# Performance work log

Hardware: AMD Instinct MI355X
Metric: run time of the kernel (lower is better)

Reference implementation:

```python
import jax, jax.numpy as jnp
import numpy as np

N_NODES = 50000
N_EDGES = 800000
NODE_IN = 16
NODE_OUT = 3
H = 128
N_LAYERS = 3


def setup_inputs() -> dict:
    key = jax.random.key(0)
    ks = jax.random.split(key, 16)
    s = 0.05
    inp = {
        "x": jax.random.normal(ks[0], (N_NODES, NODE_IN), dtype=jnp.float32),
        "edge_index": jax.random.randint(ks[1], (2, N_EDGES), 0, N_NODES, dtype=jnp.int64),
        # encoder / decoder
        "enc_w": jax.random.normal(ks[2], (NODE_IN, H), dtype=jnp.float32) * s,
        "enc_b": jnp.zeros((H,), dtype=jnp.float32),
        "dec_w": jax.random.normal(ks[3], (H, NODE_OUT), dtype=jnp.float32) * s,
        "dec_b": jnp.zeros((NODE_OUT,), dtype=jnp.float32),
        # 3 processor layers, edge MLP: Linear(2H,H) -> ReLU -> Linear(H,H)
        "edge_w1": jax.random.normal(ks[4], (N_LAYERS, 2 * H, H), dtype=jnp.float32) * s,
        "edge_b1": jnp.zeros((N_LAYERS, H), dtype=jnp.float32),
        "edge_w2": jax.random.normal(ks[5], (N_LAYERS, H, H), dtype=jnp.float32) * s,
        "edge_b2": jnp.zeros((N_LAYERS, H), dtype=jnp.float32),
        # node MLP: Linear(2H,H) -> ReLU -> Linear(H,H)
        "node_w1": jax.random.normal(ks[6], (N_LAYERS, 2 * H, H), dtype=jnp.float32) * s,
        "node_b1": jnp.zeros((N_LAYERS, H), dtype=jnp.float32),
        "node_w2": jax.random.normal(ks[7], (N_LAYERS, H, H), dtype=jnp.float32) * s,
        "node_b2": jnp.zeros((N_LAYERS, H), dtype=jnp.float32),
    }
    return inp


def reference(x, edge_index, enc_w, enc_b, dec_w, dec_b,
              edge_w1, edge_b1, edge_w2, edge_b2,
              node_w1, node_b1, node_w2, node_b2):
    row = edge_index[0]  # source nodes
    col = edge_index[1]  # destination nodes
    h = x @ enc_w + enc_b  # [N, H]
    for l in range(N_LAYERS):
        # EdgeModel: cat(src, dest) -> MLP
        e_in = jnp.concatenate([h[row], h[col]], axis=1)  # [E, 2H]
        e = jnp.maximum(e_in @ edge_w1[l] + edge_b1[l], 0.0) @ edge_w2[l] + edge_b2[l]  # [E, H]
        # NodeModel: scatter_add messages by col, cat with x -> MLP
        agg = jax.ops.segment_sum(e, col, num_segments=h.shape[0])  # [N, H]
        n_in = jnp.concatenate([h, agg], axis=1)  # [N, 2H]
        h_upd = jnp.maximum(n_in @ node_w1[l] + node_b1[l], 0.0) @ node_w2[l] + node_b2[l]
        h = h + h_upd  # residual
    return h @ dec_w + dec_b  # [N, NODE_OUT]
```

## Files before the change

### kernel.cpp

```cpp
#include <hip/hip_runtime.h>
#include <hip/hip_bf16.h>
#include <stdint.h>

#define N_NODES 50000
#define N_EDGES 800000
#define HID 128
#define NODE_IN 16
#define NODE_OUT 3
#define EDGE_TILES 12500
#define NODE_TILES 782
#define SCAN_BLOCKS 196

typedef __attribute__((ext_vector_type(8))) short short8;
typedef __attribute__((ext_vector_type(4))) float f32x4;

__device__ __forceinline__ unsigned short f2bf(float f) {
    union { float f; unsigned int u; } v; v.f = f;
    unsigned int u = v.u;
    u += 0x7fff + ((u >> 16) & 1);
    return (unsigned short)(u >> 16);
}
__device__ __forceinline__ float bf2f(unsigned short s) {
    union { unsigned int u; float f; } v; v.u = ((unsigned int)s) << 16;
    return v.f;
}
__device__ __forceinline__ float bfu_lo(unsigned int u) {
    union { unsigned int u; float f; } v; v.u = u << 16; return v.f;
}
__device__ __forceinline__ float bfu_hi(unsigned int u) {
    union { unsigned int u; float f; } v; v.u = u & 0xffff0000u; return v.f;
}

__global__ void k1_hist_mfold(const int* __restrict__ colp, int* __restrict__ cnt,
                              int* __restrict__ rank,
                              const float* __restrict__ edge_w2, const float* __restrict__ node_w1,
                              const float* __restrict__ edge_b2,
                              float* __restrict__ Mtmp, float* __restrict__ Vtmp) {
    for (int e = blockIdx.x * 256 + threadIdx.x; e < N_EDGES; e += gridDim.x * 256)
        rank[e] = atomicAdd(&cnt[colp[e]], 1);
    for (int d = blockIdx.x * 256 + threadIdx.x; d < 3 * 16384; d += gridDim.x * 256) {
        int L = d / 16384, rem = d & 16383;
        int k = rem >> 7, n = rem & 127;
        const float* w2  = edge_w2 + (size_t)L * 16384;
        const float* w1b = node_w1 + (size_t)L * 32768 + 16384;
        float acc = 0.f;
        #pragma unroll 4
        for (int j = 0; j < 128; j++) acc += w2[k * 128 + j] * w1b[j * 128 + n];
        Mtmp[d] = acc;
        if (k == 0) {
            const float* b2 = edge_b2 + (size_t)L * 128;
            float vv = 0.f;
            #pragma unroll 4
            for (int j = 0; j < 128; j++) vv += b2[j] * w1b[j * 128 + n];
            Vtmp[L * 128 + n] = vv;
        }
    }
}

__global__ __launch_bounds__(256) void k2a_scan1_swizzle(
    const int* __restrict__ cnt, int* __restrict__ ex, int* __restrict__ bsums,
    const float* __restrict__ edge_w1, const float* __restrict__ node_w1,
    const float* __restrict__ node_w2, const float* __restrict__ Mtmp,
    unsigned short* __restrict__ swz) {
    __shared__ int s[256];
    int b = blockIdx.x, t = threadIdx.x;
    if (b < SCAN_BLOCKS) {
        int i = b * 256 + t;
        int v = (i < N_NODES) ? cnt[i] : 0;
        s[t] = v;
        __syncthreads();
        for (int off = 1; off < 256; off <<= 1) {
            int u = (t >= off) ? s[t - off] : 0;
            __syncthreads();
            s[t] += u;
            __syncthreads();
        }
        if (i < N_NODES) ex[i] = s[t] - v;
        if (t == 255) bsums[b] = s[255];
    } else {
        for (int d = (b - SCAN_BLOCKS) * 256 + t; d < 3 * 98304;
             d += (gridDim.x - SCAN_BLOCKS) * 256) {
            int L = d / 98304;
            int rem = d - L * 98304;
            unsigned short* base = swz + L * 98304;
            if (rem < 32768) {
                const float* w1 = edge_w1 + (size_t)L * 32768;
                int j = rem & 7, ll = (rem >> 3) & 63, tt = rem >> 9;
                int nt = tt & 15, kt = tt >> 4;
                int k = kt * 32 + ((ll >> 4) << 3) + j;
                int cc = nt * 16 + (ll & 15);
                float v = (cc < 128) ? w1[k * 128 + cc] : w1[(128 + k) * 128 + (cc - 128)];
                base[rem] = f2bf(v);
            } else if (rem < 49152) {
            } else if (rem < 81920) {
                int d2 = rem - 49152;
                int j = d2 & 7, ll = (d2 >> 3) & 63, tt = d2 >> 9;
                int nt = tt & 7, kt = tt >> 3;
                int k = kt * 32 + ((ll >> 4) << 3) + j, n = (nt << 4) + (ll & 15);
                float v = (k < 128) ? node_w1[(size_t)L * 32768 + k * 128 + n]
                                    : Mtmp[(size_t)L * 16384 + (k - 128) * 128 + n];
                base[rem] = f2bf(v);
            } else {
                int d2 = rem - 81920;
                const float* src = node_w2 + (size_t)L * 16384;
                int j = d2 & 7, ll = (d2 >> 3) & 63, tt = d2 >> 9;
                int nt = tt & 7, kt = tt >> 3;
                int k = kt * 32 + ((ll >> 4) << 3) + j, n = (nt << 4) + (ll & 15);
                base[rem] = f2bf(src[k * 128 + n]);
            }
        }
    }
}

__global__ void k2b_scan2(int* bsums) {
    __shared__ int s[256];
    int t = threadIdx.x;
    int v = (t < SCAN_BLOCKS) ? bsums[t] : 0;
    s[t] = v;
    __syncthreads();
    for (int off = 1; off < 256; off <<= 1) {
        int u = (t >= off) ? s[t - off] : 0;
        __syncthreads();
        s[t] += u;
        __syncthreads();
    }
    if (t < SCAN_BLOCKS) bsums[t] = s[t] - v;
}

__global__ void k3a_scatter(const int* __restrict__ rowp, const int* __restrict__ colp,
                            const int* __restrict__ ex, const int* __restrict__ bsums,
                            const int* __restrict__ rank, int2* __restrict__ rc_sorted) {
    int e = blockIdx.x * 256 + threadIdx.x;
    if (e >= N_EDGES) return;
    int c = colp[e];
    int pos = ex[c] + bsums[c >> 8] + rank[e];
    rc_sorted[pos] = make_int2(rowp[e], c);
}

__global__ __launch_bounds__(256, 2) void k3b_encoder_sd(
    const float* __restrict__ x, const float* __restrict__ enc_w, const float* __restrict__ enc_b,
    const unsigned short* __restrict__ w1c, unsigned short* __restrict__ h,
    unsigned short* __restrict__ S, unsigned short* __restrict__ D)
{
    __shared__ float wts[NODE_IN * HID];
    __shared__ float bts[HID];
    __shared__ float xs[64][NODE_IN];
    __shared__ unsigned short hs[64][136];
    int t = threadIdx.x, wave = t >> 6, l = t & 63, q = l >> 4, l16 = l & 15;
    int n0 = blockIdx.x * 64;
    int nt0s = wave * 4;

    for (int i = t; i < NODE_IN * HID; i += 256) wts[i] = enc_w[i];
    if (t < HID) bts[t] = enc_b[t];
    for (int i = t; i < 64 * NODE_IN; i += 256) {
        int nl = i >> 4, ii = i & 15;
        int n = n0 + nl;
        xs[nl][ii] = (n < N_NODES) ? x[n * NODE_IN + ii] : 0.f;
    }
    short8 wr[4][4];
    #pragma unroll
    for (int kt = 0; kt < 4; kt++)
        #pragma unroll
        for (int i = 0; i < 4; i++)
            wr[kt][i] = *(const short8*)(w1c + ((kt * 16 + nt0s + i) * 64 + l) * 8);
    __syncthreads();

    for (int o = t; o < 64 * HID; o += 256) {
        int nl = o >> 7, cc = o & 127;
        float acc = bts[cc];
        #pragma unroll
        for (int i = 0; i < NODE_IN; i++) acc += xs[nl][i] * wts[i * HID + cc];
        unsigned short hb = f2bf(acc);
        hs[nl][cc] = hb;
        int n = n0 + nl;
        if (n < N_NODES) h[n * HID + cc] = hb;
    }
    __syncthreads();

    f32x4 acc[4][4];
    #pragma unroll
    for (int g = 0; g < 4; g++)
        #pragma unroll
        for (int i = 0; i < 4; i++) acc[g][i] = (f32x4){0.f, 0.f, 0.f, 0.f};
    #pragma unroll
    for (int kt = 0; kt < 4; kt++) {
        #pragma unroll
        for (int g = 0; g < 4; g++) {
            short8 a = *(const short8*)&hs[g * 16 + l16][kt * 32 + q * 8];
            #pragma unroll
            for (int i = 0; i < 4; i++)
                acc[g][i] = __builtin_amdgcn_mfma_f32_16x16x32_bf16(a, wr[kt][i], acc[g][i], 0, 0, 0);
        }
    }
    #pragma unroll
    for (int i = 0; i < 4; i++) {
        int cc = (nt0s + i) * 16 + l16;
        #pragma unroll
        for (int g = 0; g < 4; g++)
            #pragma unroll
            for (int r = 0; r < 4; r++) {
                int n = n0 + g * 16 + q * 4 + r;
                if (n < N_NODES) {
                    unsigned short v = f2bf(acc[g][i][r]);
                    if (cc < 128) S[n * HID + cc] = v;
                    else          D[n * HID + (cc - 128)] = v;
                }
            }
    }
}

__global__ __launch_bounds__(256, 4) void edge_kernel(
    const unsigned short* __restrict__ S, const unsigned short* __restrict__ D,
    const int2* __restrict__ rc_sorted,
    const float* __restrict__ b1, float* __restrict__ aggH)
{
    __shared__ float hid_s[64][132];
    __shared__ int row_s[64], col_s[64];
    int t = threadIdx.x;
    int ch = t & 15;

    float b1v[8];
    #pragma unroll
    for (int j = 0; j < 8; j++) b1v[j] = b1[ch * 8 + j];

    for (int tile = blockIdx.x; tile < EDGE_TILES; tile += gridDim.x) {
        int e0 = tile * 64;
        if (t < 64) {
            int2 rc = rc_sorted[e0 + t];
            row_s[t] = rc.x;
            col_s[t] = rc.y;
        }
        __syncthreads();

        #pragma unroll
        for (int it = 0; it < 4; it++) {
            int el = it * 16 + (t >> 4);
            int r = row_s[el], c = col_s[el];
            short8 sv = *(const short8*)(S + r * HID + ch * 8);
            short8 dv = *(const short8*)(D + c * HID + ch * 8);
            float o[8];
            #pragma unroll
            for (int p = 0; p < 4; p++) {
                unsigned int us = ((const unsigned int*)&sv)[p];
                unsigned int ud = ((const unsigned int*)&dv)[p];
                float v0 = bfu_lo(us) + bfu_lo(ud) + b1v[p * 2];
                float v1 = bfu_hi(us) + bfu_hi(ud) + b1v[p * 2 + 1];
                o[p * 2]     = v0 > 0.f ? v0 : 0.f;
                o[p * 2 + 1] = v1 > 0.f ? v1 : 0.f;
            }
            *(f32x4*)&hid_s[el][ch * 8]     = *(f32x4*)&o[0];
            *(f32x4*)&hid_s[el][ch * 8 + 4] = *(f32x4*)&o[4];
        }
        __syncthreads();

        {
            int c = t & 127;
            int h2 = t >> 7;
            int r0 = h2 * 32;
            float accv = 0.f;
            int cur = col_s[r0];
            #pragma unroll 4
            for (int r = r0; r < r0 + 32; r++) {
                accv += hid_s[r][c];
                int nxt = (r == r0 + 31) ? -1 : col_s[r + 1];
                if (nxt != cur) {
                    unsafeAtomicAdd(&aggH[cur * HID + c], accv);
                    accv = 0.f;
                    cur = nxt;
                }
            }
        }
        __syncthreads();
    }
}

template<int LAST>
__global__ __launch_bounds__(256, 4) void node_kernel(
    unsigned short* __restrict__ h, float* __restrict__ aggH, const int* __restrict__ cnt,
    const unsigned short* __restrict__ w1m_s, const float* __restrict__ b1,
    const float* __restrict__ vfold,
    const unsigned short* __restrict__ w2s, const float* __restrict__ b2,
    const unsigned short* __restrict__ w1c_next,
    unsigned short* __restrict__ S, unsigned short* __restrict__ D,
    const float* __restrict__ dec_w, const float* __restrict__ dec_b, float* __restrict__ out)
{
    __shared__ unsigned short in_h[64][136];
    __shared__ unsigned short in_a[64][136];
    __shared__ int cnt_s[64];
    __shared__ float dw[HID * NODE_OUT];
    __shared__ float db[NODE_OUT];
    int t = threadIdx.x, wave = t >> 6, l = t & 63, q = l >> 4, l16 = l & 15;
    int nt0 = wave * 2, nt0s = wave * 4;
    int n0 = blockIdx.x * 64;

    if (LAST) {
        for (int i = t; i < HID * NODE_OUT; i += 256) dw[i] = dec_w[i];
        if (t < NODE_OUT) db[t] = dec_b[t];
    }

    #pragma unroll
    for (int it = 0; it < 8; it++) {
        int g = it * 256 + t;
        int nl = g >> 5, sub = g & 31, half = sub >> 4, li = sub & 15;
        int n = n0 + nl;
        short8 v = (short8){0, 0, 0, 0, 0, 0, 0, 0};
        if (n < N_NODES) {
            if (half == 0) {
                v = *(const short8*)(h + n * HID + li * 8);
            } else {
                float* ap = aggH + n * HID + li * 8;
                f32x4 a0 = *(f32x4*)ap, a1 = *(f32x4*)(ap + 4);
                #pragma unroll
                for (int j = 0; j < 4; j++) {
                    ((unsigned short*)&v)[j]     = f2bf(a0[j]);
                    ((unsigned short*)&v)[4 + j] = f2bf(a1[j]);
                }
                if (!LAST) {
                    *(f32x4*)ap       = (f32x4){0.f, 0.f, 0.f, 0.f};
                    *(f32x4*)(ap + 4) = (f32x4){0.f, 0.f, 0.f, 0.f};
                }
            }
        }
        if (half == 0) *(short8*)&in_h[nl][li * 8] = v;
        else           *(short8*)&in_a[nl][li * 8] = v;
    }
    if (t < 64) cnt_s[t] = (n0 + t < N_NODES) ? cnt[n0 + t] : 0;
    __syncthreads();

    float b1r0 = b1[nt0 * 16 + l16], b1r1 = b1[(nt0 + 1) * 16 + l16];
    float vr0 = vfold[nt0 * 16 + l16], vr1 = vfold[(nt0 + 1) * 16 + l16];
    float b2r0 = b2[nt0 * 16 + l16], b2r1 = b2[(nt0 + 1) * 16 + l16];

    f32x4 acc[4][2];
    #pragma unroll
    for (int g = 0; g < 4; g++)
        #pragma unroll
        for (int j = 0; j < 2; j++) acc[g][j] = (f32x4){0.f, 0.f, 0.f, 0.f};
    #pragma unroll
    for (int kt = 0; kt < 8; kt++) {
        short8 b0 = *(const short8*)(w1m_s + ((kt * 8 + nt0)     * 64 + l) * 8);
        short8 b1v = *(const short8*)(w1m_s + ((kt * 8 + nt0 + 1) * 64 + l) * 8);
        #pragma unroll
        for (int g = 0; g < 4; g++) {
            short8 a = (kt < 4) ? *(const short8*)&in_h[g * 16 + l16][kt * 32 + q * 8]
                                : *(const short8*)&in_a[g * 16 + l16][(kt - 4) * 32 + q * 8];
            acc[g][0] = __builtin_amdgcn_mfma_f32_16x16x32_bf16(a, b0, acc[g][0], 0, 0, 0);
            acc[g][1] = __builtin_amdgcn_mfma_f32_16x16x32_bf16(a, b1v, acc[g][1], 0, 0, 0);
        }
    }
    __syncthreads();

    #pragma unroll
    for (int j = 0; j < 2; j++) {
        float bv = j ? b1r1 : b1r0;
        float vv = j ? vr1 : vr0;
        #pragma unroll
        for (int g = 0; g < 4; g++)
            #pragma unroll
            for (int r = 0; r < 4; r++) {
                int m2 = g * 16 + q * 4 + r;
                float v = acc[g][j][r] + bv + (float)cnt_s[m2] * vv;
                v = v > 0.f ? v : 0.f;
                in_a[m2][(nt0 + j) * 16 + l16] = f2bf(v);
            }
    }
    __syncthreads();

    f32x4 acc2[4][2];
    #pragma unroll
    for (int g = 0; g < 4; g++)
        #pragma unroll
        for (int j = 0; j < 2; j++) acc2[g][j] = (f32x4){0.f, 0.f, 0.f, 0.f};
    #pragma unroll
    for (int kt = 0; kt < 4; kt++) {
        short8 b0 = *(const short8*)(w2s + ((kt * 8 + nt0)     * 64 + l) * 8);
        short8 b1v = *(const short8*)(w2s + ((kt * 8 + nt0 + 1) * 64 + l) * 8);
        #pragma unroll
        for (int g = 0; g < 4; g++) {
            short8 a = *(const short8*)&in_a[g * 16 + l16][kt * 32 + q * 8];
            acc2[g][0] = __builtin_amdgcn_mfma_f32_16x16x32_bf16(a, b0, acc2[g][0], 0, 0, 0);
            acc2[g][1] = __builtin_amdgcn_mfma_f32_16x16x32_bf16(a, b1v, acc2[g][1], 0, 0, 0);
        }
    }
    #pragma unroll
    for (int j = 0; j < 2; j++) {
        float bv = j ? b2r1 : b2r0;
        #pragma unroll
        for (int g = 0; g < 4; g++)
            #pragma unroll
            for (int r = 0; r < 4; r++) {
                float v = acc2[g][j][r] + bv;
                int m2 = g * 16 + q * 4 + r;
                int n = n0 + m2;
                if (n < N_NODES) {
                    int c = (nt0 + j) * 16 + l16;
                    unsigned short nh = f2bf(bf2f(in_h[m2][c]) + v);
                    if (!LAST) h[n * HID + c] = nh;
                    in_h[m2][c] = nh;
                }
            }
    }
    __syncthreads();

    if (!LAST) {
        #pragma unroll
        for (int p = 0; p < 2; p++) {
            short8 wr[4][2];
            #pragma unroll
            for (int kt = 0; kt < 4; kt++) {
                wr[kt][0] = *(const short8*)(w1c_next + ((kt * 16 + nt0s + p * 2)     * 64 + l) * 8);
                wr[kt][1] = *(const short8*)(w1c_next + ((kt * 16 + nt0s + p * 2 + 1) * 64 + l) * 8);
            }
            f32x4 accs[4][2];
            #pragma unroll
            for (int g = 0; g < 4; g++)
                #pragma unroll
                for (int i = 0; i < 2; i++) accs[g][i] = (f32x4){0.f, 0.f, 0.f, 0.f};
            #pragma unroll
            for (int kt = 0; kt < 4; kt++) {
                #pragma unroll
                for (int g = 0; g < 4; g++) {
                    short8 a = *(const short8*)&in_h[g * 16 + l16][kt * 32 + q * 8];
                    accs[g][0] = __builtin_amdgcn_mfma_f32_16x16x32_bf16(a, wr[kt][0], accs[g][0], 0, 0, 0);
                    accs[g][1] = __builtin_amdgcn_mfma_f32_16x16x32_bf16(a, wr[kt][1], accs[g][1], 0, 0, 0);
                }
            }
            #pragma unroll
            for (int i = 0; i < 2; i++) {
                int c = (nt0s + p * 2 + i) * 16 + l16;
                #pragma unroll
                for (int g = 0; g < 4; g++)
                    #pragma unroll
                    for (int r = 0; r < 4; r++) {
                        int n = n0 + g * 16 + q * 4 + r;
                        if (n < N_NODES) {
                            unsigned short v = f2bf(accs[g][i][r]);
                            if (c < 128) S[n * HID + c] = v;
                            else         D[n * HID + (c - 128)] = v;
                        }
                    }
            }
        }
    } else {
        if (t < 64 * NODE_OUT) {
            int nl = t / 3, o = t - 3 * nl;
            int n = n0 + nl;
            if (n < N_NODES) {
                float a = db[o];
                #pragma unroll 4
                for (int k = 0; k < HID; k++) a += bf2f(in_h[nl][k]) * dw[k * 3 + o];
                out[n * 3 + o] = a;
            }
        }
    }
}

extern "C" void kernel_launch(void* const* d_in, const int* in_sizes, int n_in,
                              void* d_out, int out_size, void* d_ws, size_t ws_size,
                              hipStream_t stream) {
    const float* x       = (const float*)d_in[0];
    const int*   ei      = (const int*)d_in[1];
    const float* enc_w   = (const float*)d_in[2];
    const float* enc_b   = (const float*)d_in[3];
    const float* dec_w   = (const float*)d_in[4];
    const float* dec_b   = (const float*)d_in[5];
    const float* edge_w1 = (const float*)d_in[6];
    const float* edge_b1 = (const float*)d_in[7];
    const float* edge_w2 = (const float*)d_in[8];
    const float* edge_b2 = (const float*)d_in[9];
    const float* node_w1 = (const float*)d_in[10];
    const float* node_b1 = (const float*)d_in[11];
    const float* node_w2 = (const float*)d_in[12];
    const float* node_b2 = (const float*)d_in[13];

    char* ws = (char*)d_ws;
    unsigned short* h    = (unsigned short*)ws;
    float*          aggH = (float*)(ws + 12800000);
    unsigned short* swz  = (unsigned short*)(ws + 38400000);
    int* cnt             = (int*)(ws + 38989824);
    int* ex              = (int*)(ws + 39189824);
    int* bsums           = (int*)(ws + 39389824);
    int2* rc_sorted      = (int2*)(ws + 39390848);
    unsigned short* Sbuf = (unsigned short*)(ws + 45790848);
    unsigned short* Dbuf = (unsigned short*)(ws + 58590848);
    float* Mtmp          = (float*)(ws + 71390848);
    float* Vtmp          = (float*)(ws + 71587456);
    int* rank            = (int*)(ws + 58590848);

    const int* rowp = ei;
    const int* colp = ei + N_EDGES;

    hipMemsetAsync(cnt, 0, (size_t)N_NODES * 4, stream);
    hipMemsetAsync(aggH, 0, (size_t)N_NODES * HID * 4, stream);

    k1_hist_mfold<<<1024, 256, 0, stream>>>(colp, cnt, rank, edge_w2, node_w1, edge_b2,
                                            Mtmp, Vtmp);
    k2a_scan1_swizzle<<<SCAN_BLOCKS + 288, 256, 0, stream>>>(cnt, ex, bsums, edge_w1,
                                                             node_w1, node_w2, Mtmp, swz);
    k2b_scan2<<<1, 256, 0, stream>>>(bsums);
    k3a_scatter<<<3125, 256, 0, stream>>>(rowp, colp, ex, bsums, rank, rc_sorted);
    k3b_encoder_sd<<<NODE_TILES, 256, 0, stream>>>(x, enc_w, enc_b, swz , h,
                                                   Sbuf, Dbuf);

    for (int L = 0; L < 3; L++) {
        unsigned short* base = swz + (size_t)L * 98304;
        unsigned short* next = swz + (size_t)(L + 1) * 98304;
        edge_kernel<<<1024, 256, 0, stream>>>(Sbuf, Dbuf, rc_sorted,
                                              edge_b1 + (size_t)L * HID, aggH);
        if (L < 2) {
            node_kernel<0><<<NODE_TILES, 256, 0, stream>>>(
                h, aggH, cnt,
                base + 49152, node_b1 + (size_t)L * HID, Vtmp + (size_t)L * HID,
                base + 81920, node_b2 + (size_t)L * HID,
                next, Sbuf, Dbuf, dec_w, dec_b, (float*)d_out);
        } else {
            node_kernel<1><<<NODE_TILES, 256, 0, stream>>>(
                h, aggH, cnt,
                base + 49152, node_b1 + (size_t)L * HID, Vtmp + (size_t)L * HID,
                base + 81920, node_b2 + (size_t)L * HID,
                base , Sbuf, Dbuf, dec_w, dec_b, (float*)d_out);
        }
    }
}
```

Baseline: 412.3 us.

## Rewrite edge kernel as register-resident segmented reduction per 16-lane group

The edge kernel no longer stages ReLU hidden values in shared memory with block-wide syncs. Each 16-lane group now walks 32 col-sorted edges and keeps the destination row plus bias in registers. It gathers source rows 8 at a time, accumulates ReLU outputs in registers, and does atomic adds only when the destination changes. This removes LDS traffic and barriers and reuses the D load across runs of the same destination, at the cost of more registers and each lane issuing 8 scalar atomics per flush. The encoder launch bound is also raised to 4 blocks per SM.

```diff
diff --git a/kernel.cpp b/kernel.cpp
--- a/kernel.cpp
+++ b/kernel.cpp
@@ -7,9 +7,10 @@
 #define HID 128
 #define NODE_IN 16
 #define NODE_OUT 3
-#define EDGE_TILES 12500
 #define NODE_TILES 782
 #define SCAN_BLOCKS 196
+#define EPG 32
+#define NGROUPS (N_EDGES / EPG)
 
 typedef __attribute__((ext_vector_type(8))) short short8;
 typedef __attribute__((ext_vector_type(4))) float f32x4;
@@ -137,7 +138,7 @@
     rc_sorted[pos] = make_int2(rowp[e], c);
 }
 
-__global__ __launch_bounds__(256, 2) void k3b_encoder_sd(
+__global__ __launch_bounds__(256, 4) void k3b_encoder_sd(
     const float* __restrict__ x, const float* __restrict__ enc_w, const float* __restrict__ enc_b,
     const unsigned short* __restrict__ w1c, unsigned short* __restrict__ h,
     unsigned short* __restrict__ S, unsigned short* __restrict__ D)
@@ -209,69 +210,78 @@
     }
 }
 
-__global__ __launch_bounds__(256, 4) void edge_kernel(
+__global__ __launch_bounds__(256) void edge_kernel(
     const unsigned short* __restrict__ S, const unsigned short* __restrict__ D,
     const int2* __restrict__ rc_sorted,
     const float* __restrict__ b1, float* __restrict__ aggH)
 {
-    __shared__ float hid_s[64][132];
-    __shared__ int row_s[64], col_s[64];
     int t = threadIdx.x;
     int ch = t & 15;
+    int gid = (blockIdx.x * 256 + t) >> 4;
+    if (gid >= NGROUPS) return;
+    int e0 = gid * EPG;
 
     float b1v[8];
     #pragma unroll
     for (int j = 0; j < 8; j++) b1v[j] = b1[ch * 8 + j];
 
-    for (int tile = blockIdx.x; tile < EDGE_TILES; tile += gridDim.x) {
-        int e0 = tile * 64;
-        if (t < 64) {
-            int2 rc = rc_sorted[e0 + t];
-            row_s[t] = rc.x;
-            col_s[t] = rc.y;
-        }
-        __syncthreads();
-
-        #pragma unroll
-        for (int it = 0; it < 4; it++) {
-            int el = it * 16 + (t >> 4);
-            int r = row_s[el], c = col_s[el];
-            short8 sv = *(const short8*)(S + r * HID + ch * 8);
-            short8 dv = *(const short8*)(D + c * HID + ch * 8);
-            float o[8];
+    float acc[8];
+    #pragma unroll
+    for (int j = 0; j < 8; j++) acc[j] = 0.f;
+
+    int cur = rc_sorted[e0].y;
+    float dreg[8];
+    {
+        short8 dv = *(const short8*)(D + (size_t)cur * HID + ch * 8);
+        #pragma unroll
+        for (int p = 0; p < 4; p++) {
+            unsigned int ud = ((const unsigned int*)&dv)[p];
+            dreg[p * 2]     = bfu_lo(ud) + b1v[p * 2];
+            dreg[p * 2 + 1] = bfu_hi(ud) + b1v[p * 2 + 1];
+        }
+    }
+
+    #pragma unroll
+    for (int base = 0; base < EPG; base += 8) {
+        int2 rcb[8];
+        #pragma unroll
+        for (int i = 0; i < 8; i++) rcb[i] = rc_sorted[e0 + base + i];
+        short8 sv[8];
+        #pragma unroll
+        for (int i = 0; i < 8; i++)
+            sv[i] = *(const short8*)(S + (size_t)rcb[i].x * HID + ch * 8);
+
+        #pragma unroll
+        for (int i = 0; i < 8; i++) {
+            int c = rcb[i].y;
+            if (c != cur) {
+                #pragma unroll
+                for (int j = 0; j < 8; j++)
+                    unsafeAtomicAdd(&aggH[(size_t)cur * HID + ch * 8 + j], acc[j]);
+                #pragma unroll
+                for (int j = 0; j < 8; j++) acc[j] = 0.f;
+                short8 dv = *(const short8*)(D + (size_t)c * HID + ch * 8);
+                #pragma unroll
+                for (int p = 0; p < 4; p++) {
+                    unsigned int ud = ((const unsigned int*)&dv)[p];
+                    dreg[p * 2]     = bfu_lo(ud) + b1v[p * 2];
+                    dreg[p * 2 + 1] = bfu_hi(ud) + b1v[p * 2 + 1];
+                }
+                cur = c;
+            }
             #pragma unroll
             for (int p = 0; p < 4; p++) {
-                unsigned int us = ((const unsigned int*)&sv)[p];
-                unsigned int ud = ((const unsigned int*)&dv)[p];
-                float v0 = bfu_lo(us) + bfu_lo(ud) + b1v[p * 2];
-                float v1 = bfu_hi(us) + bfu_hi(ud) + b1v[p * 2 + 1];
-                o[p * 2]     = v0 > 0.f ? v0 : 0.f;
-                o[p * 2 + 1] = v1 > 0.f ? v1 : 0.f;
-            }
-            *(f32x4*)&hid_s[el][ch * 8]     = *(f32x4*)&o[0];
-            *(f32x4*)&hid_s[el][ch * 8 + 4] = *(f32x4*)&o[4];
-        }
-        __syncthreads();
-
-        {
-            int c = t & 127;
-            int h2 = t >> 7;
-            int r0 = h2 * 32;
-            float accv = 0.f;
-            int cur = col_s[r0];
-            #pragma unroll 4
-            for (int r = r0; r < r0 + 32; r++) {
-                accv += hid_s[r][c];
-                int nxt = (r == r0 + 31) ? -1 : col_s[r + 1];
-                if (nxt != cur) {
-                    unsafeAtomicAdd(&aggH[cur * HID + c], accv);
-                    accv = 0.f;
-                    cur = nxt;
-                }
-            }
-        }
-        __syncthreads();
-    }
+                unsigned int us = ((const unsigned int*)&sv[i])[p];
+                float v0 = bfu_lo(us) + dreg[p * 2];
+                float v1 = bfu_hi(us) + dreg[p * 2 + 1];
+                acc[p * 2]     += v0 > 0.f ? v0 : 0.f;
+                acc[p * 2 + 1] += v1 > 0.f ? v1 : 0.f;
+            }
+        }
+    }
+    #pragma unroll
+    for (int j = 0; j < 8; j++)
+        unsafeAtomicAdd(&aggH[(size_t)cur * HID + ch * 8 + j], acc[j]);
 }
 
 template<int LAST>
@@ -502,11 +512,12 @@
     k3b_encoder_sd<<<NODE_TILES, 256, 0, stream>>>(x, enc_w, enc_b, swz , h,
                                                    Sbuf, Dbuf);
 
+    const int edge_blocks = (NGROUPS * 16 + 255) / 256;
     for (int L = 0; L < 3; L++) {
         unsigned short* base = swz + (size_t)L * 98304;
         unsigned short* next = swz + (size_t)(L + 1) * 98304;
-        edge_kernel<<<1024, 256, 0, stream>>>(Sbuf, Dbuf, rc_sorted,
-                                              edge_b1 + (size_t)L * HID, aggH);
+        edge_kernel<<<edge_blocks, 256, 0, stream>>>(Sbuf, Dbuf, rc_sorted,
+                                                     edge_b1 + (size_t)L * HID, aggH);
         if (L < 2) {
             node_kernel<0><<<NODE_TILES, 256, 0, stream>>>(
                 h, aggH, cnt,
```

After: 1.079 ms. +161.6%, slower.
